# Kernel optimization log

Hardware: AMD Instinct MI355X
Metric: run time of the kernel (lower is better)

## Reference

```python
import jax, jax.numpy as jnp
import numpy as np

B, C, T, H, W, TS = 4, 512, 2048, 8, 16, 1000
D = C // H  # head_dim = 64
SCALE = D ** -0.5


def _conv1x1(w, b, z):
    # torch Conv1d(dim, dim, 1): (B,C,T) -> (B,C,T)
    return jnp.einsum('oc,bct->bot', w, z) + b[None, :, None]


def _linear(w, b, z):
    # torch Linear: z @ w.T + b, w is (out,in)
    return z @ w.T + b


def _rope(x, cos, sin):
    # x: (B,H,T,D); cos/sin: (T, D//2) broadcast over (B,H)
    x1, x2 = x[..., ::2], x[..., 1::2]
    r = jnp.stack([x1 * cos - x2 * sin, x1 * sin + x2 * cos], axis=-1)
    return r.reshape(x.shape)


def _local(x, cond, qw, qb, kw, kb, vw, vb, ow, ob):
    q = _conv1x1(qw, qb, x)
    k = _conv1x1(kw, kb, cond)
    v = _conv1x1(vw, vb, cond)
    pl = W // 2
    pr = W - pl - 1
    kp = jnp.pad(k, ((0, 0), (0, 0), (pl, pr)))
    vp = jnp.pad(v, ((0, 0), (0, 0), (pl, pr)))
    idx = jnp.arange(T)[:, None] + jnp.arange(W)[None, :]  # (T,W)
    ku = kp[:, :, idx].reshape(B, H, D, T, W)
    vu = vp[:, :, idx].reshape(B, H, D, T, W)
    qh = q.reshape(B, H, D, T)
    dots = jnp.einsum('bhdt,bhdtw->bhtw', qh, ku) * SCALE
    attn = jax.nn.softmax(dots, axis=-1)
    out = jnp.einsum('bhtw,bhdtw->bhdt', attn, vu)
    # faithful to torch: permute(0,1,3,2).contiguous().view(B,C,T)
    out = out.transpose(0, 1, 3, 2).reshape(B, C, T)
    return _conv1x1(ow, ob, out)


def _global(xg, cg, qw, qb, kw, kb, vw, vb, ow, ob):
    # xg, cg: (B,T,C)
    q = _linear(qw, qb, xg).reshape(B, T, H, D).transpose(0, 2, 1, 3)
    k = _linear(kw, kb, cg).reshape(B, T, H, D).transpose(0, 2, 1, 3)
    v = _linear(vw, vb, cg).reshape(B, T, H, D).transpose(0, 2, 1, 3)
    inv_freq = 1.0 / (10000.0 ** (jnp.arange(0, D, 2, dtype=jnp.float32) / D))
    pos = jnp.arange(T, dtype=jnp.float32)
    sinus = pos[:, None] * inv_freq[None, :]  # (T, D//2)
    cos, sin = jnp.cos(sinus), jnp.sin(sinus)
    q = _rope(q, cos, sin)
    k = _rope(k, cos, sin)
    dots = jnp.einsum('bhqd,bhkd->bhqk', q, k) * SCALE
    attn = jax.nn.softmax(dots, axis=-1)
    out = jnp.einsum('bhqk,bhkd->bhqd', attn, v)
    out = out.transpose(0, 2, 1, 3).reshape(B, T, C)
    return _linear(ow, ob, out)


def setup_inputs() -> dict:
    key = jax.random.key(0)
    ks = jax.random.split(key, 20)
    pm = lambda k: jax.random.normal(k, (C, C), dtype=jnp.float32) * 0.02
    pb = lambda k: jax.random.normal(k, (C,), dtype=jnp.float32) * 0.02
    return {
        'x': jax.random.normal(ks[0], (B, C, T), dtype=jnp.float32),
        'cond': jax.random.normal(ks[1], (B, C, T), dtype=jnp.float32),
        't': jax.random.randint(ks[2], (B,), 0, TS),
        'lq_w': pm(ks[3]), 'lq_b': pb(ks[4]),
        'lk_w': pm(ks[5]), 'lk_b': pb(ks[6]),
        'lv_w': pm(ks[7]), 'lv_b': pb(ks[8]),
        'lo_w': pm(ks[9]), 'lo_b': pb(ks[10]),
        'gq_w': pm(ks[11]), 'gq_b': pb(ks[12]),
        'gk_w': pm(ks[13]), 'gk_b': pb(ks[14]),
        'gv_w': pm(ks[15]), 'gv_b': pb(ks[16]),
        'go_w': pm(ks[17]), 'go_b': pb(ks[18]),
    }


def reference(x, cond, t, lq_w, lq_b, lk_w, lk_b, lv_w, lv_b, lo_w, lo_b,
              gq_w, gq_b, gk_w, gk_b, gv_w, gv_b, go_w, go_b):
    ctx_local = _local(x, cond, lq_w, lq_b, lk_w, lk_b, lv_w, lv_b, lo_w, lo_b)
    ctx_global = _global(x.transpose(0, 2, 1), cond.transpose(0, 2, 1),
                         gq_w, gq_b, gk_w, gk_b, gv_w, gv_b, go_w, go_b)
    ctx_global = ctx_global.transpose(0, 2, 1)  # (B,C,T)
    t_norm = t.astype(jnp.float32) / jnp.float32(TS - 1)
    a_g = (1.0 - t_norm)[:, None, None]
    a_l = t_norm[:, None, None]
    return jnp.sqrt(a_g) * ctx_global + jnp.sqrt(a_l) * ctx_local
```

## Files before the change

### kernel.cpp

```cpp
#include <hip/hip_runtime.h>
#include <math.h>

#define BB 4
#define CC 512
#define TT 2048
#define HH 8
#define DD 64

static constexpr float SCALE = 0.125f;
static constexpr float QK_SCALE_LOG2 = 0.125f * 1.4426950408889634f;

typedef __attribute__((ext_vector_type(8)))  short  short8;
typedef __attribute__((ext_vector_type(4)))  float  f32x4;
typedef __attribute__((ext_vector_type(16))) float  f32x16;
typedef __attribute__((ext_vector_type(2)))  unsigned int u32x2;

static __device__ __forceinline__ ushort f2bf(float f) {
    uint u = __float_as_uint(f);
    uint r = (u + 0x7fffu + ((u >> 16) & 1u)) >> 16;
    return (ushort)r;
}
static __device__ __forceinline__ float bf2f(ushort u) {
    return __uint_as_float((uint)u << 16);
}

typedef unsigned int u32;
typedef u32 __attribute__((address_space(1))) gu32;
typedef u32 __attribute__((address_space(3))) lu32;
static __device__ __forceinline__ void gload_lds16(const void* g, void* l) {
    __builtin_amdgcn_global_load_lds((const gu32*)g, (lu32*)l, 16, 0, 0);
}

__global__ __launch_bounds__(256)
void prep_kernel(const float* __restrict__ x, const float* __restrict__ cond,
                 const float* w0, const float* w1, const float* w2, const float* w3,
                 const float* w4, const float* w5, const float* w6, const float* w7,
                 ushort* __restrict__ wbf, ushort* __restrict__ wc,
                 ushort* __restrict__ xtb, ushort* __restrict__ ctb,
                 float* __restrict__ ctab, float* __restrict__ stab)
{
    __shared__ ushort L[64][66];
    int bid = blockIdx.x;
    const int tid = threadIdx.x;

    if (bid < 256) {
        int idx = bid * 256 + tid;
        int i = idx >> 11;
        int t = idx & 2047;
        float ex   = (2.0f * (float)i) / 64.0f;
        float invf = powf(10000.0f, -ex);
        float ang  = (float)t * invf;
        ctab[idx] = cosf(ang);
        stab[idx] = sinf(ang);
        return;
    }
    bid -= 256;
    if (bid < 2048) {
        const float* srcs[8] = {w0, w1, w2, w3, w4, w5, w6, w7};
        int wi = bid >> 8;
        int idx = ((bid & 255) * 256 + tid) * 4;
        float4 v = *(const float4*)&srcs[wi][idx];
        uint lo = (uint)f2bf(v.x) | ((uint)f2bf(v.y) << 16);
        uint hi = (uint)f2bf(v.z) | ((uint)f2bf(v.w) << 16);
        uint2 pk = make_uint2(lo, hi);
        if (wi < 6) {
            *(uint2*)&wbf[(size_t)wi * 262144 + idx] = pk;
        } else {
            int row = idx >> 9, col = idx & 511;
            *(uint2*)&wc[(size_t)row * 1024 + (wi - 6) * 512 + col] = pk;
        }
        return;
    }
    bid -= 2048;
    const int z = bid >> 8;
    const int r = bid & 255;
    const float* in = (z < 4) ? x : cond;
    ushort* outp    = (z < 4) ? xtb : ctb;
    const int b = z & 3;
    const int t0 = (r & 31) * 64, c0 = (r >> 5) * 64;
    const float* inb = in + (size_t)b * CC * TT;
    ushort* outb = outp + (size_t)b * TT * CC;
    const int lc = tid >> 6;
    const int lt = tid & 63;
    #pragma unroll
    for (int i = 0; i < 16; i++) {
        int c = i * 4 + lc;
        L[c][lt] = f2bf(inb[(size_t)(c0 + c) * TT + t0 + lt]);
    }
    __syncthreads();
    #pragma unroll
    for (int i = 0; i < 16; i++) {
        int t = i * 4 + lc;
        outb[(size_t)(t0 + t) * CC + c0 + lt] = L[lt][t];
    }
}

__global__ __launch_bounds__(256)
void transpose_bf16_kernel(const ushort* __restrict__ in, ushort* __restrict__ AG)
{
    __shared__ ushort L[64][66];
    const int t0 = blockIdx.x * 64, c0 = blockIdx.y * 64, b = blockIdx.z;
    const ushort* inb = in + (size_t)b * CC * TT;
    ushort* outb = AG + (size_t)b * TT * 1024;
    const int lc = threadIdx.x >> 6;
    const int lt = threadIdx.x & 63;
    #pragma unroll
    for (int i = 0; i < 16; i++) {
        int c = i * 4 + lc;
        L[c][lt] = inb[(size_t)(c0 + c) * TT + t0 + lt];
    }
    __syncthreads();
    #pragma unroll
    for (int i = 0; i < 16; i++) {
        int t = i * 4 + lc;
        outb[(size_t)(t0 + t) * 1024 + c0 + lt] = L[lt][t];
    }
}

#define GEMM_BODY(Wp, XTp, KD, NB)                                                  \
    __shared__ __align__(16) ushort As[2][128][32];                                 \
    __shared__ __align__(16) ushort Bs[2][NB][32];                                  \
    const int tid  = threadIdx.x;                                                   \
    const int wid  = tid >> 6;                                                      \
    const int lane = tid & 63;                                                      \
    const int x  = lane & 15;                                                       \
    const int gq = lane >> 4;                                                       \
    const int wm = wid >> 1, wn = wid & 1;                                          \
    const int m0 = blockIdx.y * 128;                                                \
    const int n0 = blockIdx.x * NB;                                                 \
    const int srow = lane >> 2;                                                     \
    const int sblk = lane & 3;                                                      \
    f32x4 acc[4][NB / 32];                                                          \
    _Pragma("unroll")                                                               \
    for (int i = 0; i < 4; i++)                                                     \
        _Pragma("unroll")                                                           \
        for (int j = 0; j < NB / 32; j++) acc[i][j] = (f32x4){0.f, 0.f, 0.f, 0.f};  \
    auto stage = [&](int bf, int k0) {                                              \
        _Pragma("unroll")                                                           \
        for (int c = 0; c < 2; c++) {                                               \
            int row = c * 64 + wid * 16 + srow;                                     \
            int dbk = sblk ^ ((row >> 1) & 3);                                      \
            gload_lds16(&Wp[(size_t)(m0 + row) * KD + k0 + dbk * 8],                \
                        &As[bf][c * 64 + wid * 16][0]);                             \
            if (c * 64 < NB)                                                        \
                gload_lds16(&XTp[(size_t)(n0 + row) * KD + k0 + dbk * 8],           \
                            &Bs[bf][c * 64 + wid * 16][0]);                         \
        }                                                                           \
    };                                                                              \
    stage(0, 0);                                                                    \
    __syncthreads();                                                                \
    for (int ks = 0; ks < (KD) / 32; ks++) {                                        \
        int cur = ks & 1;                                                           \
        if (ks < (KD) / 32 - 1) stage(cur ^ 1, (ks + 1) * 32);                      \
        short8 aF[4], bF[NB / 32];                                                  \
        _Pragma("unroll")                                                           \
        for (int mi = 0; mi < 4; mi++) {                                            \
            int row = wm * 64 + mi * 16 + x;                                        \
            aF[mi] = *(const short8*)&As[cur][row][(gq ^ ((row >> 1) & 3)) * 8];    \
        }                                                                           \
        _Pragma("unroll")                                                           \
        for (int nj = 0; nj < NB / 32; nj++) {                                      \
            int row = wn * (NB / 2) + nj * 16 + x;                                  \
            bF[nj] = *(const short8*)&Bs[cur][row][(gq ^ ((row >> 1) & 3)) * 8];    \
        }                                                                           \
        _Pragma("unroll")                                                           \
        for (int mi = 0; mi < 4; mi++)                                              \
            _Pragma("unroll")                                                       \
            for (int nj = 0; nj < NB / 32; nj++)                                    \
                acc[mi][nj] = __builtin_amdgcn_mfma_f32_16x16x32_bf16(aF[mi], bF[nj], acc[mi][nj], 0, 0, 0); \
        __syncthreads();                                                            \
    }

__global__ __launch_bounds__(256)
void gemm6_kernel(const ushort* __restrict__ wbase,
                  const float* __restrict__ b0, const float* __restrict__ b1, const float* __restrict__ b2,
                  const float* __restrict__ b3, const float* __restrict__ b4, const float* __restrict__ b5,
                  const ushort* __restrict__ xtb, const ushort* __restrict__ ctb,
                  ushort* __restrict__ y0, ushort* __restrict__ y1, ushort* __restrict__ y2,
                  ushort* __restrict__ y3, ushort* __restrict__ y4, ushort* __restrict__ y5,
                  const float* __restrict__ ctab, const float* __restrict__ stab)
{
    const int z = blockIdx.z;
    const ushort* Wp  = wbase + (size_t)z * 262144;
    const float* bias = (z == 0) ? b0 : (z == 1) ? b1 : (z == 2) ? b2 : (z == 3) ? b3 : (z == 4) ? b4 : b5;
    const ushort* XTp = (z == 0 || z == 3) ? xtb : ctb;
    ushort* Y = (z == 0) ? y0 : (z == 1) ? y1 : (z == 2) ? y2 : (z == 3) ? y3 : (z == 4) ? y4 : y5;
    const bool do_rope = (z == 3 || z == 4);
    const float qscale = (z == 3) ? QK_SCALE_LOG2 : 1.0f;

    GEMM_BODY(Wp, XTp, 512, 128)

    const int bidx = (n0 + wn * 64) >> 11;
    #pragma unroll
    for (int mi = 0; mi < 4; mi++) {
        const int mb = m0 + wm * 64 + mi * 16 + 4 * gq;
        float bv[4];
        #pragma unroll
        for (int r = 0; r < 4; r++) bv[r] = bias[mb + r];
        #pragma unroll
        for (int nj = 0; nj < 4; nj++) {
            const int n  = n0 + wn * 64 + nj * 16 + x;
            const int tt = n & 2047;
            f32x4 v = acc[mi][nj];
            v[0] += bv[0]; v[1] += bv[1]; v[2] += bv[2]; v[3] += bv[3];
            if (do_rope) {
                const int i0 = (mb & 63) >> 1;
                float c0 = ctab[(size_t)i0 * 2048 + tt],       s0 = stab[(size_t)i0 * 2048 + tt];
                float c1 = ctab[(size_t)(i0 + 1) * 2048 + tt], s1 = stab[(size_t)(i0 + 1) * 2048 + tt];
                float e0 = (v[0] * c0 - v[1] * s0) * qscale;
                float e1 = (v[0] * s0 + v[1] * c0) * qscale;
                float e2 = (v[2] * c1 - v[3] * s1) * qscale;
                float e3 = (v[2] * s1 + v[3] * c1) * qscale;
                v[0] = e0; v[1] = e1; v[2] = e2; v[3] = e3;
            }
            if (z <= 3) {
                uint lo = (uint)f2bf(v[0]) | ((uint)f2bf(v[1]) << 16);
                uint hi = (uint)f2bf(v[2]) | ((uint)f2bf(v[3]) << 16);
                *(uint2*)&Y[(size_t)n * 512 + mb] = make_uint2(lo, hi);
            } else if (z == 4) {
                const int hh = (mb >> 6) & 7;
                const int d  = mb & 63;
                const int kap = d >> 4, hb = (d >> 3) & 1, j0 = d & 7;
                const int kt = tt >> 6, tk = tt & 63, sb = tk >> 5, qh = tk & 31;
                size_t off = ((size_t)(bidx * 8 + hh)) * 131072
                           + (size_t)(((((kt * 2 + sb) * 4 + kap) * 2 + hb) * 32 + qh) * 8 + j0);
                uint lo = (uint)f2bf(v[0]) | ((uint)f2bf(v[1]) << 16);
                uint hi = (uint)f2bf(v[2]) | ((uint)f2bf(v[3]) << 16);
                *(uint2*)&Y[off] = make_uint2(lo, hi);
            } else {
                const int hh = (mb >> 6) & 7;
                const int qh0 = mb & 31, db = (mb & 63) >> 5;
                const int kt = tt >> 6, kk = tt & 63;
                const int kc = kk >> 4, hb = (kk >> 3) & 1, j = kk & 7;
                size_t base = ((size_t)(bidx * 8 + hh)) * 131072
                            + (size_t)(((((kt * 2 + db) * 4 + kc) * 2 + hb) * 32 + qh0) * 8 + j);
                #pragma unroll
                for (int r = 0; r < 4; r++)
                    Y[base + (size_t)r * 8] = f2bf(v[r]);
            }
        }
    }
}

__global__ __launch_bounds__(256)
void gemm_comb_kernel(const ushort* __restrict__ Wp,
                      const float* __restrict__ bl, const float* __restrict__ bg,
                      const ushort* __restrict__ XTp, float* __restrict__ Y,
                      const int* __restrict__ tarr)
{
    GEMM_BODY(Wp, XTp, 1024, 64)

    const int bidx = (n0 + wn * 32) >> 11;
    float tn = (float)tarr[bidx] / 999.0f;
    float sl = sqrtf(tn), sg = sqrtf(1.0f - tn);

    #pragma unroll
    for (int mi = 0; mi < 4; mi++) {
        const int mb = m0 + wm * 64 + mi * 16 + 4 * gq;
        float bv[4];
        #pragma unroll
        for (int r = 0; r < 4; r++) bv[r] = sl * bl[mb + r] + sg * bg[mb + r];
        #pragma unroll
        for (int nj = 0; nj < 2; nj++) {
            const int tt = (n0 + wn * 32 + nj * 16 + x) & 2047;
            f32x4 v = acc[mi][nj];
            #pragma unroll
            for (int r = 0; r < 4; r++)
                Y[((size_t)bidx * 512 + mb + r) * 2048 + tt] = v[r] + bv[r];
        }
    }
}

__global__ __launch_bounds__(256)
void local_attn_kernel(const ushort* __restrict__ qt, const ushort* __restrict__ kt,
                       const ushort* __restrict__ vt, ushort* __restrict__ outb,
                       const int* __restrict__ tarr)
{
    int gidx = blockIdx.x * 256 + threadIdx.x;
    int t  = gidx & (TT - 1);
    int bh = gidx >> 11;
    int h  = bh & (HH - 1);
    int b  = bh >> 3;
    const size_t rb = (size_t)b * TT;
    const int co = h * DD;
    const float wl = sqrtf((float)tarr[b] / 999.0f);

    float qf[64];
    {
        const ushort* qp = qt + (rb + t) * 512 + co;
        #pragma unroll
        for (int i = 0; i < 8; i++) {
            short8 v = *(const short8*)&qp[i * 8];
            #pragma unroll
            for (int j = 0; j < 8; j++) qf[i * 8 + j] = bf2f((ushort)v[j]);
        }
    }

    int koff[16]; float msk[16];
    #pragma unroll
    for (int w = 0; w < 16; w++) {
        int kidx = t + w - 8;
        msk[w]  = (kidx >= 0 && kidx < TT) ? 1.0f : 0.0f;
        koff[w] = min(max(kidx, 0), TT - 1);
    }

    float dots[16];
    #pragma unroll
    for (int w = 0; w < 16; w++) {
        const ushort* kp = kt + (rb + koff[w]) * 512 + co;
        float d0 = 0.f, d1 = 0.f;
        #pragma unroll
        for (int i = 0; i < 8; i++) {
            short8 v = *(const short8*)&kp[i * 8];
            #pragma unroll
            for (int j = 0; j < 8; j += 2) {
                d0 = fmaf(qf[i * 8 + j],     bf2f((ushort)v[j]),     d0);
                d1 = fmaf(qf[i * 8 + j + 1], bf2f((ushort)v[j + 1]), d1);
            }
        }
        dots[w] = d0 + d1;
    }

    float m = -1e30f;
    #pragma unroll
    for (int w = 0; w < 16; w++) { dots[w] = dots[w] * SCALE * msk[w]; m = fmaxf(m, dots[w]); }
    float p[16], s = 0.f;
    #pragma unroll
    for (int w = 0; w < 16; w++) { p[w] = __expf(dots[w] - m); s += p[w]; }
    float inv = wl / s;
    #pragma unroll
    for (int w = 0; w < 16; w++) p[w] *= msk[w] * inv;

    float oa[64];
    #pragma unroll
    for (int d = 0; d < 64; d++) oa[d] = 0.f;
    #pragma unroll
    for (int w = 0; w < 16; w++) {
        const ushort* vp = vt + (rb + koff[w]) * 512 + co;
        #pragma unroll
        for (int i = 0; i < 8; i++) {
            short8 v = *(const short8*)&vp[i * 8];
            #pragma unroll
            for (int j = 0; j < 8; j++)
                oa[i * 8 + j] = fmaf(p[w], bf2f((ushort)v[j]), oa[i * 8 + j]);
        }
    }

    ushort* op = outb + ((size_t)b * CC + co + (t >> 5)) * TT + (size_t)(t & 31) * DD;
    #pragma unroll
    for (int i = 0; i < 16; i++) {
        uint lo = (uint)f2bf(oa[i * 4 + 0]) | ((uint)f2bf(oa[i * 4 + 1]) << 16);
        uint hi = (uint)f2bf(oa[i * 4 + 2]) | ((uint)f2bf(oa[i * 4 + 3]) << 16);
        *(uint2*)&op[i * 4] = make_uint2(lo, hi);
    }
}

__global__ __launch_bounds__(256)
void flash_global_kernel(const ushort* __restrict__ qtd, const ushort* __restrict__ KT,
                         const ushort* __restrict__ VT, ushort* __restrict__ AG,
                         const int* __restrict__ tarr)
{
    __shared__ __align__(16) ushort Ks[2][4096];
    __shared__ __align__(16) ushort Vs[2][4096];

    const int tid  = threadIdx.x;
    const int w    = tid >> 6;
    const int lane = tid & 63;
    const int qh   = lane & 31;
    const int h    = lane >> 5;

    const int bid = blockIdx.x;
    const int sw  = (bid & 7) * 64 + (bid >> 3);
    const int qt  = sw & 15;
    const int p   = sw >> 4;
    const int hh  = p & 7, b = p >> 3;

    const size_t kvbase = (size_t)p * 131072;
    const size_t btd    = (size_t)b * TT;
    const int q_glob = qt * 128 + w * 32 + qh;
    const float sg_mix = sqrtf(1.0f - (float)tarr[b] / 999.0f);

    const ushort* Kb = KT + kvbase;
    const ushort* Vb = VT + kvbase;

    short8 aQ[4];
    {
        const ushort* qrow = qtd + (btd + q_glob) * 512 + hh * 64;
        #pragma unroll
        for (int kap = 0; kap < 4; kap++)
            aQ[kap] = *(const short8*)&qrow[kap * 16 + h * 8];
    }

    f32x16 oacc[2];
    #pragma unroll
    for (int d = 0; d < 2; d++)
        #pragma unroll
        for (int r = 0; r < 16; r++) oacc[d][r] = 0.f;
    float l_run = 0.0f;

    const ushort* kA = Kb + (size_t)(2 * w) * 512 + lane * 8;
    const ushort* vA = Vb + (size_t)(2 * w) * 512 + lane * 8;

    auto issue = [&](int buf, int kt) {
        const size_t off = (size_t)kt * 4096;
        gload_lds16(kA + off,       &Ks[buf][(2 * w) * 512]);
        gload_lds16(kA + off + 512, &Ks[buf][(2 * w + 1) * 512]);
        gload_lds16(vA + off,       &Vs[buf][(2 * w) * 512]);
        gload_lds16(vA + off + 512, &Vs[buf][(2 * w + 1) * 512]);
    };
    issue(0, 0);

    int cur = 0;
    for (int kt = 0; kt < 32; kt++) {
        __syncthreads();
        if (kt < 31) issue(cur ^ 1, kt + 1);

        const ushort* KsC = &Ks[cur][0];
        const ushort* VsC = &Vs[cur][0];

        f32x16 ST[2];
        #pragma unroll
        for (int sb = 0; sb < 2; sb++)
            #pragma unroll
            for (int r = 0; r < 16; r++) ST[sb][r] = 0.f;
        __builtin_amdgcn_s_setprio(1);
        #pragma unroll
        for (int sb = 0; sb < 2; sb++)
            #pragma unroll
            for (int kap = 0; kap < 4; kap++) {
                short8 aK = *(const short8*)&KsC[(sb * 4 + kap) * 512 + lane * 8];
                ST[sb] = __builtin_amdgcn_mfma_f32_32x32x16_bf16(aK, aQ[kap], ST[sb], 0, 0, 0);
            }
        __builtin_amdgcn_s_setprio(0);

        float s0 = 0.f, s1 = 0.f, s2 = 0.f, s3 = 0.f;
        #pragma unroll
        for (int sb = 0; sb < 2; sb++)
            #pragma unroll
            for (int r = 0; r < 16; r += 4) {
                ST[sb][r + 0] = __builtin_amdgcn_exp2f(ST[sb][r + 0]);
                ST[sb][r + 1] = __builtin_amdgcn_exp2f(ST[sb][r + 1]);
                ST[sb][r + 2] = __builtin_amdgcn_exp2f(ST[sb][r + 2]);
                ST[sb][r + 3] = __builtin_amdgcn_exp2f(ST[sb][r + 3]);
                s0 += ST[sb][r + 0]; s1 += ST[sb][r + 1];
                s2 += ST[sb][r + 2]; s3 += ST[sb][r + 3];
            }
        l_run += (s0 + s1) + (s2 + s3);

        short8 bP[4];
        #pragma unroll
        for (int sb = 0; sb < 2; sb++)
            #pragma unroll
            for (int kcp = 0; kcp < 2; kcp++) {
                const int rb2 = kcp * 8;
                uint ca, cb, cc, cd;
                asm("v_cvt_pk_bf16_f32 %0, %1, %2" : "=v"(ca) : "v"(ST[sb][rb2 + 0]), "v"(ST[sb][rb2 + 1]));
                asm("v_cvt_pk_bf16_f32 %0, %1, %2" : "=v"(cb) : "v"(ST[sb][rb2 + 2]), "v"(ST[sb][rb2 + 3]));
                asm("v_cvt_pk_bf16_f32 %0, %1, %2" : "=v"(cc) : "v"(ST[sb][rb2 + 4]), "v"(ST[sb][rb2 + 5]));
                asm("v_cvt_pk_bf16_f32 %0, %1, %2" : "=v"(cd) : "v"(ST[sb][rb2 + 6]), "v"(ST[sb][rb2 + 7]));
                u32x2 r1 = __builtin_amdgcn_permlane32_swap(ca, cc, false, false);
                u32x2 r2 = __builtin_amdgcn_permlane32_swap(cb, cd, false, false);
                uint4 bu = make_uint4(r1[0], r2[0], r1[1], r2[1]);
                bP[sb * 2 + kcp] = __builtin_bit_cast(short8, bu);
            }

        __builtin_amdgcn_s_setprio(1);
        #pragma unroll
        for (int db = 0; db < 2; db++)
            #pragma unroll
            for (int kc = 0; kc < 4; kc++) {
                short8 aV = *(const short8*)&VsC[(db * 4 + kc) * 512 + lane * 8];
                oacc[db] = __builtin_amdgcn_mfma_f32_32x32x16_bf16(aV, bP[kc], oacc[db], 0, 0, 0);
            }
        __builtin_amdgcn_s_setprio(0);
        cur ^= 1;
    }

    float ltot = l_run + __shfl_xor(l_run, 32);
    float inv = sg_mix / ltot;
    ushort* agrow = AG + (btd + q_glob) * 1024 + 512 + hh * 64;
    #pragma unroll
    for (int db = 0; db < 2; db++)
        #pragma unroll
        for (int rq = 0; rq < 4; rq++) {
            const int d0 = db * 32 + rq * 8 + h * 4;
            uint lo = (uint)f2bf(oacc[db][rq * 4 + 0] * inv) | ((uint)f2bf(oacc[db][rq * 4 + 1] * inv) << 16);
            uint hi = (uint)f2bf(oacc[db][rq * 4 + 2] * inv) | ((uint)f2bf(oacc[db][rq * 4 + 3] * inv) << 16);
            *(uint2*)&agrow[d0] = make_uint2(lo, hi);
        }
}

extern "C" void kernel_launch(void* const* d_in, const int* in_sizes, int n_in,
                              void* d_out, int out_size, void* d_ws, size_t ws_size,
                              hipStream_t stream)
{
    const float* x    = (const float*)d_in[0];
    const float* cond = (const float*)d_in[1];
    const int*   tarr = (const int*)d_in[2];
    const float* lq_w = (const float*)d_in[3];
    const float* lq_b = (const float*)d_in[4];
    const float* lk_w = (const float*)d_in[5];
    const float* lk_b = (const float*)d_in[6];
    const float* lv_w = (const float*)d_in[7];
    const float* lv_b = (const float*)d_in[8];
    const float* lo_w = (const float*)d_in[9];
    const float* lo_b = (const float*)d_in[10];
    const float* gq_w = (const float*)d_in[11];
    const float* gq_b = (const float*)d_in[12];
    const float* gk_w = (const float*)d_in[13];
    const float* gk_b = (const float*)d_in[14];
    const float* gv_w = (const float*)d_in[15];
    const float* gv_b = (const float*)d_in[16];
    const float* go_w = (const float*)d_in[17];
    const float* go_b = (const float*)d_in[18];
    float* out = (float*)d_out;

    const size_t N = (size_t)BB * CC * TT;
    char* w = (char*)d_ws;
    ushort* xtb = (ushort*)w; w += N * 2;
    ushort* ctb = (ushort*)w; w += N * 2;
    ushort* lq  = (ushort*)w; w += N * 2;
    ushort* lk  = (ushort*)w; w += N * 2;
    ushort* lv  = (ushort*)w; w += N * 2;
    ushort* gqb = (ushort*)w; w += N * 2;
    ushort* ktb = (ushort*)w; w += N * 2;
    ushort* vtb = (ushort*)w; w += N * 2;
    ushort* scr = (ushort*)w; w += N * 2;
    ushort* AG  = (ushort*)w; w += (size_t)BB * TT * 1024 * 2;
    ushort* wbf = (ushort*)w; w += (size_t)6 * 512 * 512 * 2;
    ushort* wc  = (ushort*)w; w += (size_t)512 * 1024 * 2;
    float* ctab = (float*)w;  w += (size_t)32 * 2048 * 4;
    float* stab = (float*)w;

    dim3 blk(256);

    prep_kernel<<<dim3(4352), blk, 0, stream>>>(x, cond,
                                                lq_w, lk_w, lv_w, gq_w, gk_w, gv_w, lo_w, go_w,
                                                wbf, wc, xtb, ctb, ctab, stab);

    gemm6_kernel<<<dim3(64, 4, 6), blk, 0, stream>>>(wbf, lq_b, lk_b, lv_b, gq_b, gk_b, gv_b,
                                                     xtb, ctb, lq, lk, lv, gqb, ktb, vtb, ctab, stab);

    local_attn_kernel<<<dim3(BB * HH * TT / 256), blk, 0, stream>>>(lq, lk, lv, scr, tarr);
    transpose_bf16_kernel<<<dim3(32, 8, BB), blk, 0, stream>>>(scr, AG);

    flash_global_kernel<<<dim3(512), blk, 0, stream>>>(gqb, ktb, vtb, AG, tarr);

    gemm_comb_kernel<<<dim3(128, 4), blk, 0, stream>>>(wc, lo_b, go_b, AG, out, tarr);
}
```

Measured before the change: 177.5 us.

## Split global flash attention over two KV halves and add a combine kernel

The global flash attention kernel now splits the key/value sequence into two halves on a second grid dimension. This doubles the block count to 1024 and halves each block's loop length. Each half writes unnormalized fp32 partial outputs and row sums into reused workspace buffers. A new combine kernel then adds them, applies the normalization and time mix, and writes bf16 into AG. The goal is better occupancy and latency hiding on the CUs, at the cost of extra fp32 partial-result traffic and one more kernel launch.

```diff
diff --git a/kernel.cpp b/kernel.cpp
--- a/kernel.cpp
+++ b/kernel.cpp
@@ -357,8 +357,9 @@
 
 __global__ __launch_bounds__(256)
 void flash_global_kernel(const ushort* __restrict__ qtd, const ushort* __restrict__ KT,
-                         const ushort* __restrict__ VT, ushort* __restrict__ AG,
-                         const int* __restrict__ tarr)
+                         const ushort* __restrict__ VT,
+                         float* __restrict__ PO0, float* __restrict__ PO1,
+                         float* __restrict__ L0, float* __restrict__ L1)
 {
     __shared__ __align__(16) ushort Ks[2][4096];
     __shared__ __align__(16) ushort Vs[2][4096];
@@ -369,16 +370,20 @@
     const int qh   = lane & 31;
     const int h    = lane >> 5;
 
+    const int half = blockIdx.y;
+    float* __restrict__ PO = half ? PO1 : PO0;
+    float* __restrict__ Lp = half ? L1 : L0;
+
     const int bid = blockIdx.x;
     const int sw  = (bid & 7) * 64 + (bid >> 3);
     const int qt  = sw & 15;
     const int p   = sw >> 4;
     const int hh  = p & 7, b = p >> 3;
 
-    const size_t kvbase = (size_t)p * 131072;
+    const size_t kvbase = (size_t)p * 131072 + (size_t)half * 16 * 4096;
     const size_t btd    = (size_t)b * TT;
     const int q_glob = qt * 128 + w * 32 + qh;
-    const float sg_mix = sqrtf(1.0f - (float)tarr[b] / 999.0f);
+    const int pq = p * 2048 + q_glob;
 
     const ushort* Kb = KT + kvbase;
     const ushort* Vb = VT + kvbase;
@@ -411,9 +416,9 @@
     issue(0, 0);
 
     int cur = 0;
-    for (int kt = 0; kt < 32; kt++) {
+    for (int kt = 0; kt < 16; kt++) {
         __syncthreads();
-        if (kt < 31) issue(cur ^ 1, kt + 1);
+        if (kt < 15) issue(cur ^ 1, kt + 1);
 
         const ushort* KsC = &Ks[cur][0];
         const ushort* VsC = &Vs[cur][0];
@@ -477,17 +482,34 @@
     }
 
     float ltot = l_run + __shfl_xor(l_run, 32);
-    float inv = sg_mix / ltot;
-    ushort* agrow = AG + (btd + q_glob) * 1024 + 512 + hh * 64;
+    if (h == 0) Lp[pq] = ltot;
+    float* prow = PO + (size_t)pq * 64;
     #pragma unroll
     for (int db = 0; db < 2; db++)
         #pragma unroll
         for (int rq = 0; rq < 4; rq++) {
             const int d0 = db * 32 + rq * 8 + h * 4;
-            uint lo = (uint)f2bf(oacc[db][rq * 4 + 0] * inv) | ((uint)f2bf(oacc[db][rq * 4 + 1] * inv) << 16);
-            uint hi = (uint)f2bf(oacc[db][rq * 4 + 2] * inv) | ((uint)f2bf(oacc[db][rq * 4 + 3] * inv) << 16);
-            *(uint2*)&agrow[d0] = make_uint2(lo, hi);
-        }
+            *(float4*)&prow[d0] = make_float4(oacc[db][rq * 4 + 0], oacc[db][rq * 4 + 1],
+                                              oacc[db][rq * 4 + 2], oacc[db][rq * 4 + 3]);
+        }
+}
+
+__global__ __launch_bounds__(256)
+void flash_combine_kernel(const float* __restrict__ PO0, const float* __restrict__ PO1,
+                          const float* __restrict__ L0, const float* __restrict__ L1,
+                          ushort* __restrict__ AG, const int* __restrict__ tarr)
+{
+    int idx = blockIdx.x * 256 + threadIdx.x;
+    int pq = idx >> 4;
+    int dq = (idx & 15) * 4;
+    float4 a = *(const float4*)&PO0[(size_t)pq * 64 + dq];
+    float4 c = *(const float4*)&PO1[(size_t)pq * 64 + dq];
+    float l = L0[pq] + L1[pq];
+    int b = pq >> 14, hh = (pq >> 11) & 7, t = pq & 2047;
+    float inv = sqrtf(1.0f - (float)tarr[b] / 999.0f) / l;
+    uint lo = (uint)f2bf((a.x + c.x) * inv) | ((uint)f2bf((a.y + c.y) * inv) << 16);
+    uint hi = (uint)f2bf((a.z + c.z) * inv) | ((uint)f2bf((a.w + c.w) * inv) << 16);
+    *(uint2*)&AG[(size_t)(b * 2048 + t) * 1024 + 512 + hh * 64 + dq] = make_uint2(lo, hi);
 }
 
 extern "C" void kernel_launch(void* const* d_in, const int* in_sizes, int n_in,
@@ -532,6 +554,11 @@
     float* ctab = (float*)w;  w += (size_t)32 * 2048 * 4;
     float* stab = (float*)w;
 
+    float* PO0 = (float*)xtb;
+    float* PO1 = (float*)lq;
+    float* L0  = (float*)lv;
+    float* L1  = L0 + 65536;
+
     dim3 blk(256);
 
     prep_kernel<<<dim3(4352), blk, 0, stream>>>(x, cond,
@@ -544,7 +571,8 @@
     local_attn_kernel<<<dim3(BB * HH * TT / 256), blk, 0, stream>>>(lq, lk, lv, scr, tarr);
     transpose_bf16_kernel<<<dim3(32, 8, BB), blk, 0, stream>>>(scr, AG);
 
-    flash_global_kernel<<<dim3(512), blk, 0, stream>>>(gqb, ktb, vtb, AG, tarr);
+    flash_global_kernel<<<dim3(512, 2), blk, 0, stream>>>(gqb, ktb, vtb, PO0, PO1, L0, L1);
+    flash_combine_kernel<<<dim3(4096), blk, 0, stream>>>(PO0, PO1, L0, L1, AG, tarr);
 
     gemm_comb_kernel<<<dim3(128, 4), blk, 0, stream>>>(wc, lo_b, go_b, AG, out, tarr);
 }
```

New measurement: 184.4 us. +3.9%, slower.

## Stage projection GEMM epilogue through LDS for coalesced 16-byte stores

Applied to the files above, without the earlier changes.

The macro GEMM body in the six-way projection kernel is replaced with an inlined version that shares its LDS buffer with the epilogue. Results are written into swizzled LDS and then stored as coalesced 16-byte chunks, both for the plain layouts and for the permuted K/V attention layouts. The z==5 (V) case swaps the MFMA operands so the output is transposed in registers, which avoids the previous scattered 2-byte stores. The cost is an extra LDS round trip and a barrier in the epilogue.

```diff
diff --git a/kernel.cpp b/kernel.cpp
--- a/kernel.cpp
+++ b/kernel.cpp
@@ -180,64 +180,171 @@
                   ushort* __restrict__ y3, ushort* __restrict__ y4, ushort* __restrict__ y5,
                   const float* __restrict__ ctab, const float* __restrict__ stab)
 {
+    __shared__ __align__(16) ushort SMEM[16384];
+    ushort (*As)[128][32] = (ushort(*)[128][32])&SMEM[0];
+    ushort (*Bs)[128][32] = (ushort(*)[128][32])&SMEM[8192];
+
     const int z = blockIdx.z;
     const ushort* Wp  = wbase + (size_t)z * 262144;
     const float* bias = (z == 0) ? b0 : (z == 1) ? b1 : (z == 2) ? b2 : (z == 3) ? b3 : (z == 4) ? b4 : b5;
     const ushort* XTp = (z == 0 || z == 3) ? xtb : ctb;
     ushort* Y = (z == 0) ? y0 : (z == 1) ? y1 : (z == 2) ? y2 : (z == 3) ? y3 : (z == 4) ? y4 : y5;
     const bool do_rope = (z == 3 || z == 4);
+    const bool swp = (z == 5);
     const float qscale = (z == 3) ? QK_SCALE_LOG2 : 1.0f;
 
-    GEMM_BODY(Wp, XTp, 512, 128)
-
-    const int bidx = (n0 + wn * 64) >> 11;
-    #pragma unroll
-    for (int mi = 0; mi < 4; mi++) {
-        const int mb = m0 + wm * 64 + mi * 16 + 4 * gq;
-        float bv[4];
-        #pragma unroll
-        for (int r = 0; r < 4; r++) bv[r] = bias[mb + r];
+    const int tid  = threadIdx.x;
+    const int wid  = tid >> 6;
+    const int lane = tid & 63;
+    const int x  = lane & 15;
+    const int gq = lane >> 4;
+    const int wm = wid >> 1, wn = wid & 1;
+    const int m0 = blockIdx.y * 128;
+    const int n0 = blockIdx.x * 128;
+    const int srow = lane >> 2;
+    const int sblk = lane & 3;
+
+    f32x4 acc[4][4];
+    #pragma unroll
+    for (int i = 0; i < 4; i++)
+        #pragma unroll
+        for (int j = 0; j < 4; j++) acc[i][j] = (f32x4){0.f, 0.f, 0.f, 0.f};
+
+    auto stage = [&](int bf, int k0) {
+        #pragma unroll
+        for (int c = 0; c < 2; c++) {
+            int row = c * 64 + wid * 16 + srow;
+            int dbk = sblk ^ ((row >> 1) & 3);
+            gload_lds16(&Wp[(size_t)(m0 + row) * 512 + k0 + dbk * 8],
+                        &As[bf][c * 64 + wid * 16][0]);
+            gload_lds16(&XTp[(size_t)(n0 + row) * 512 + k0 + dbk * 8],
+                        &Bs[bf][c * 64 + wid * 16][0]);
+        }
+    };
+    stage(0, 0);
+    __syncthreads();
+
+    for (int ks = 0; ks < 16; ks++) {
+        int cur = ks & 1;
+        if (ks < 15) stage(cur ^ 1, (ks + 1) * 32);
+        short8 aF[4], bF[4];
+        #pragma unroll
+        for (int mi = 0; mi < 4; mi++) {
+            int row = wm * 64 + mi * 16 + x;
+            aF[mi] = *(const short8*)&As[cur][row][(gq ^ ((row >> 1) & 3)) * 8];
+        }
         #pragma unroll
         for (int nj = 0; nj < 4; nj++) {
-            const int n  = n0 + wn * 64 + nj * 16 + x;
-            const int tt = n & 2047;
-            f32x4 v = acc[mi][nj];
-            v[0] += bv[0]; v[1] += bv[1]; v[2] += bv[2]; v[3] += bv[3];
-            if (do_rope) {
-                const int i0 = (mb & 63) >> 1;
-                float c0 = ctab[(size_t)i0 * 2048 + tt],       s0 = stab[(size_t)i0 * 2048 + tt];
-                float c1 = ctab[(size_t)(i0 + 1) * 2048 + tt], s1 = stab[(size_t)(i0 + 1) * 2048 + tt];
-                float e0 = (v[0] * c0 - v[1] * s0) * qscale;
-                float e1 = (v[0] * s0 + v[1] * c0) * qscale;
-                float e2 = (v[2] * c1 - v[3] * s1) * qscale;
-                float e3 = (v[2] * s1 + v[3] * c1) * qscale;
-                v[0] = e0; v[1] = e1; v[2] = e2; v[3] = e3;
-            }
-            if (z <= 3) {
+            int row = wn * 64 + nj * 16 + x;
+            bF[nj] = *(const short8*)&Bs[cur][row][(gq ^ ((row >> 1) & 3)) * 8];
+        }
+        if (swp) {
+            #pragma unroll
+            for (int mi = 0; mi < 4; mi++)
+                #pragma unroll
+                for (int nj = 0; nj < 4; nj++)
+                    acc[mi][nj] = __builtin_amdgcn_mfma_f32_16x16x32_bf16(bF[nj], aF[mi], acc[mi][nj], 0, 0, 0);
+        } else {
+            #pragma unroll
+            for (int mi = 0; mi < 4; mi++)
+                #pragma unroll
+                for (int nj = 0; nj < 4; nj++)
+                    acc[mi][nj] = __builtin_amdgcn_mfma_f32_16x16x32_bf16(aF[mi], bF[nj], acc[mi][nj], 0, 0, 0);
+        }
+        __syncthreads();
+    }
+
+    if (!swp) {
+        #pragma unroll
+        for (int mi = 0; mi < 4; mi++) {
+            const int cL = wm * 64 + mi * 16 + 4 * gq;
+            const int mb = m0 + cL;
+            float bv[4];
+            #pragma unroll
+            for (int r = 0; r < 4; r++) bv[r] = bias[mb + r];
+            #pragma unroll
+            for (int nj = 0; nj < 4; nj++) {
+                const int tL = wn * 64 + nj * 16 + x;
+                const int tt = (n0 + tL) & 2047;
+                f32x4 v = acc[mi][nj];
+                v[0] += bv[0]; v[1] += bv[1]; v[2] += bv[2]; v[3] += bv[3];
+                if (do_rope) {
+                    const int i0 = (mb & 63) >> 1;
+                    float c0 = ctab[(size_t)i0 * 2048 + tt],       s0 = stab[(size_t)i0 * 2048 + tt];
+                    float c1 = ctab[(size_t)(i0 + 1) * 2048 + tt], s1 = stab[(size_t)(i0 + 1) * 2048 + tt];
+                    float e0 = (v[0] * c0 - v[1] * s0) * qscale;
+                    float e1 = (v[0] * s0 + v[1] * c0) * qscale;
+                    float e2 = (v[2] * c1 - v[3] * s1) * qscale;
+                    float e3 = (v[2] * s1 + v[3] * c1) * qscale;
+                    v[0] = e0; v[1] = e1; v[2] = e2; v[3] = e3;
+                }
                 uint lo = (uint)f2bf(v[0]) | ((uint)f2bf(v[1]) << 16);
                 uint hi = (uint)f2bf(v[2]) | ((uint)f2bf(v[3]) << 16);
-                *(uint2*)&Y[(size_t)n * 512 + mb] = make_uint2(lo, hi);
-            } else if (z == 4) {
-                const int hh = (mb >> 6) & 7;
-                const int d  = mb & 63;
-                const int kap = d >> 4, hb = (d >> 3) & 1, j0 = d & 7;
-                const int kt = tt >> 6, tk = tt & 63, sb = tk >> 5, qh = tk & 31;
-                size_t off = ((size_t)(bidx * 8 + hh)) * 131072
-                           + (size_t)(((((kt * 2 + sb) * 4 + kap) * 2 + hb) * 32 + qh) * 8 + j0);
-                uint lo = (uint)f2bf(v[0]) | ((uint)f2bf(v[1]) << 16);
-                uint hi = (uint)f2bf(v[2]) | ((uint)f2bf(v[3]) << 16);
-                *(uint2*)&Y[off] = make_uint2(lo, hi);
-            } else {
-                const int hh = (mb >> 6) & 7;
-                const int qh0 = mb & 31, db = (mb & 63) >> 5;
-                const int kt = tt >> 6, kk = tt & 63;
-                const int kc = kk >> 4, hb = (kk >> 3) & 1, j = kk & 7;
-                size_t base = ((size_t)(bidx * 8 + hh)) * 131072
-                            + (size_t)(((((kt * 2 + db) * 4 + kc) * 2 + hb) * 32 + qh0) * 8 + j);
-                #pragma unroll
-                for (int r = 0; r < 4; r++)
-                    Y[base + (size_t)r * 8] = f2bf(v[r]);
+                const int blk = (cL >> 3) ^ (tL & 7);
+                *(uint2*)&SMEM[tL * 128 + blk * 8 + (gq & 1) * 4] = make_uint2(lo, hi);
             }
+        }
+    } else {
+        #pragma unroll
+        for (int mi = 0; mi < 4; mi++) {
+            const int cL = wm * 64 + mi * 16 + x;
+            const float bv = bias[m0 + cL];
+            #pragma unroll
+            for (int nj = 0; nj < 4; nj++) {
+                const int tL = wn * 64 + nj * 16 + 4 * gq;
+                f32x4 v = acc[mi][nj];
+                uint lo = (uint)f2bf(v[0] + bv) | ((uint)f2bf(v[1] + bv) << 16);
+                uint hi = (uint)f2bf(v[2] + bv) | ((uint)f2bf(v[3] + bv) << 16);
+                const int blk = (tL >> 3) ^ (cL & 7);
+                *(uint2*)&SMEM[cL * 128 + blk * 8 + (gq & 1) * 4] = make_uint2(lo, hi);
+            }
+        }
+    }
+    __syncthreads();
+
+    if (z <= 3) {
+        #pragma unroll
+        for (int s = 0; s < 8; s++) {
+            const int chunk = s * 256 + tid;
+            const int row = chunk >> 4;
+            const int blk = chunk & 15;
+            uint4 val = *(const uint4*)&SMEM[row * 128 + ((blk ^ (row & 7)) << 3)];
+            *(uint4*)&Y[(size_t)(n0 + row) * 512 + m0 + blk * 8] = val;
+        }
+    } else if (z == 4) {
+        const int bidx = n0 >> 11;
+        #pragma unroll
+        for (int s = 0; s < 8; s++) {
+            const int chunk = s * 256 + tid;
+            const int row = chunk & 127;
+            const int blk = chunk >> 7;
+            uint4 val = *(const uint4*)&SMEM[row * 128 + ((blk ^ (row & 7)) << 3)];
+            const int tt = (n0 + row) & 2047;
+            const int kt = tt >> 6, tk = tt & 63, sb = tk >> 5, qh = tk & 31;
+            const int c = m0 + blk * 8;
+            const int hh = (c >> 6) & 7, d = c & 63;
+            const int kap = d >> 4, hb = (d >> 3) & 1;
+            size_t off = (size_t)(bidx * 8 + hh) * 131072
+                       + (size_t)(((((kt * 2 + sb) * 4 + kap) * 2 + hb) * 32 + qh) * 8);
+            *(uint4*)&Y[off] = val;
+        }
+    } else {
+        const int bidx = n0 >> 11;
+        #pragma unroll
+        for (int s = 0; s < 8; s++) {
+            const int chunk = s * 256 + tid;
+            const int rowc = chunk & 127;
+            const int blk = chunk >> 7;
+            uint4 val = *(const uint4*)&SMEM[rowc * 128 + ((blk ^ (rowc & 7)) << 3)];
+            const int c = m0 + rowc;
+            const int hh = (c >> 6) & 7, d = c & 63;
+            const int qh = d & 31, db = (d >> 5) & 1;
+            const int tt0 = (n0 + blk * 8) & 2047;
+            const int kt = tt0 >> 6, kk = tt0 & 63;
+            const int kc = kk >> 4, hb = (kk >> 3) & 1;
+            size_t off = (size_t)(bidx * 8 + hh) * 131072
+                       + (size_t)(((((kt * 2 + db) * 4 + kc) * 2 + hb) * 32 + qh) * 8);
+            *(uint4*)&Y[off] = val;
         }
     }
 }
```

After: 173.9 us. 1.02x faster.
